# Optimization experiments

Measured on AMD Instinct MI355X. Metric: run time of the kernel, lower is better.

## Reference

```python
import jax, jax.numpy as jnp
import numpy as np

N_NODES = 50000
N_EDGES = 800000
FEATS = 128
HIDDEN = 64
CLASSES = 64


def graph_conv(x, edges):
    """GCN-style symmetric-normalized aggregation over an edge list (no self-loops;
    self information is supplied via the concat in the host module)."""
    src, dst = edges[0], edges[1]
    ones = jnp.ones((edges.shape[1],), dtype=x.dtype)
    deg = jax.ops.segment_sum(ones, dst, num_segments=N_NODES)
    inv_sqrt = jax.lax.rsqrt(jnp.maximum(deg, 1.0))
    coef = inv_sqrt[src] * inv_sqrt[dst]            # [E]
    msg = x[src] * coef[:, None]                     # [E, H] gather
    return jax.ops.segment_sum(msg, dst, num_segments=N_NODES)  # [N, H] scatter


def setup_inputs() -> dict:
    key = jax.random.key(0)
    ks = jax.random.split(key, 16)
    def lin(k, out_d, in_d):
        return jax.random.normal(k, (out_d, in_d), dtype=jnp.float32) / np.sqrt(in_d)
    x = jax.random.normal(ks[0], (N_NODES, FEATS), dtype=jnp.float32)
    edges = jax.random.randint(ks[1], (2, N_EDGES), 0, N_NODES, dtype=jnp.int64)
    return {
        "x": x,
        "edges": edges,
        "W1": lin(ks[2], HIDDEN, FEATS),
        "b1": jnp.zeros((HIDDEN,), dtype=jnp.float32),
        "W2": lin(ks[3], HIDDEN, 2 * HIDDEN),
        "A2a": lin(ks[4], HIDDEN, HIDDEN),
        "A2b": lin(ks[5], HIDDEN, HIDDEN),
        "W3": lin(ks[6], HIDDEN, 2 * HIDDEN),
        "A3a": lin(ks[7], HIDDEN, HIDDEN),
        "A3b": lin(ks[8], HIDDEN, HIDDEN),
        "W4": lin(ks[9], CLASSES, 2 * HIDDEN),
        "A4a": lin(ks[10], CLASSES, HIDDEN),
        "A4b": lin(ks[11], CLASSES, HIDDEN),
    }


def _block(x, edges, W, Aa, Ab):
    # relu(Linear(cat[x, conv(x)]) + att_a(x) * att_b(x))
    h = graph_conv(x, edges)
    cat = jnp.concatenate([x, h], axis=1)            # [N, 2H]
    return jax.nn.relu(cat @ W.T + (x @ Aa.T) * (x @ Ab.T))


def reference(x, edges, W1, b1, W2, A2a, A2b, W3, A3a, A3b, W4, A4a, A4b):
    x = jax.nn.relu(x @ W1.T + b1)                   # [N, H]
    x = _block(x, edges, W2, A2a, A2b)               # [N, H]
    x = _block(x, edges, W3, A3a, A3b)               # [N, H]
    x = _block(x, edges, W4, A4a, A4b)               # [N, C]
    return x
```

## Files before the change

kernel.cpp:

```cpp
#include <hip/hip_runtime.h>
#include <hip/hip_bf16.h>
#include <hip/hip_fp16.h>

#define N_NODES 50000
#define N_EDGES 800000
#define NTILES 3125
#define W_TOTAL 57344
#define WB2 192
#define SCAT 512
#define TB 782
#define ROWCAP 64
#define ZROW N_NODES

typedef __attribute__((ext_vector_type(8))) short bf16x8;
typedef __attribute__((ext_vector_type(4))) float f32x4;
typedef __attribute__((ext_vector_type(2))) float f32x2;
typedef __attribute__((ext_vector_type(8))) unsigned short u16x8;
typedef __attribute__((ext_vector_type(4))) unsigned int u32x4;

__device__ inline unsigned short f2bf(float f) {
    unsigned int x = __float_as_uint(f);
    unsigned int r = (x + 0x7FFF + ((x >> 16) & 1)) >> 16;
    return (unsigned short)r;
}
__device__ inline float2 h2f2(unsigned int u) {
    __half2 h = *(__half2*)&u;
    return make_float2(__low2float(h), __high2float(h));
}
__device__ inline unsigned int f22h2(float a, float b) {
    __half2 h = __floats2half2_rn(a, b);
    return *(unsigned int*)&h;
}

__global__ __launch_bounds__(256) void pass1_kernel(
    const float* __restrict__ x, const int* __restrict__ src, const int* __restrict__ dst,
    const float* __restrict__ W1, const float* __restrict__ b1,
    const float* W2, const float* A2a, const float* A2b,
    const float* W3, const float* A3a, const float* A3b,
    const float* W4, const float* A4a, const float* A4b,
    int* __restrict__ cnt, unsigned short* __restrict__ srcAp,
    unsigned short* __restrict__ wp, __half* __restrict__ Ht) {
    int tid = threadIdx.x;

    if (blockIdx.x < SCAT) {
        for (int e = blockIdx.x * 256 + tid; e < N_EDGES; e += SCAT * 256) {
            int d = dst[e];
            int pos = atomicAdd(&cnt[d], 1);
            if (pos < ROWCAP) srcAp[(size_t)d * ROWCAP + pos] = (unsigned short)src[e];
        }
        return;
    }
    if (blockIdx.x >= SCAT + TB) {
        int i = 8192 + (blockIdx.x - SCAT - TB) * 256 + tid;
        if (i >= W_TOTAL) return;
        float v;
        if (i < 16384)      v = W2[i - 8192];
        else if (i < 20480) v = A2a[i - 16384];
        else if (i < 24576) v = A2b[i - 20480];
        else if (i < 32768) v = W3[i - 24576];
        else if (i < 36864) v = A3a[i - 32768];
        else if (i < 40960) v = A3b[i - 36864];
        else if (i < 49152) v = W4[i - 40960];
        else if (i < 53248) v = A4a[i - 49152];
        else                v = A4b[i - 53248];
        wp[i] = f2bf(v);
        return;
    }

    int wave = ((blockIdx.x - SCAT) * 256 + tid) >> 6;
    if (wave >= NTILES) return;
    int lane = tid & 63;
    int r16 = lane & 15, quad = lane >> 4;
    int base = wave * 16;

    bf16x8 a[4];
    const float* xr = x + (size_t)(base + r16) * 128 + quad * 8;
#pragma unroll
    for (int kb = 0; kb < 4; kb++) {
        float4 f0 = *(const float4*)(xr + kb * 32);
        float4 f1 = *(const float4*)(xr + kb * 32 + 4);
        bf16x8 v;
        v[0] = (short)f2bf(f0.x); v[1] = (short)f2bf(f0.y);
        v[2] = (short)f2bf(f0.z); v[3] = (short)f2bf(f0.w);
        v[4] = (short)f2bf(f1.x); v[5] = (short)f2bf(f1.y);
        v[6] = (short)f2bf(f1.z); v[7] = (short)f2bf(f1.w);
        a[kb] = v;
    }

#pragma unroll
    for (int jt = 0; jt < 4; jt++) {
        f32x4 acc = {0.f, 0.f, 0.f, 0.f};
        const float* wr = W1 + (size_t)(jt * 16 + r16) * 128 + quad * 8;
#pragma unroll
        for (int kb = 0; kb < 4; kb++) {
            float4 g0 = *(const float4*)(wr + kb * 32);
            float4 g1 = *(const float4*)(wr + kb * 32 + 4);
            bf16x8 b;
            b[0] = (short)f2bf(g0.x); b[1] = (short)f2bf(g0.y);
            b[2] = (short)f2bf(g0.z); b[3] = (short)f2bf(g0.w);
            b[4] = (short)f2bf(g1.x); b[5] = (short)f2bf(g1.y);
            b[6] = (short)f2bf(g1.z); b[7] = (short)f2bf(g1.w);
            acc = __builtin_amdgcn_mfma_f32_16x16x32_bf16(a[kb], b, acc, 0, 0, 0);
        }
        int col = jt * 16 + r16;
        float bias = b1[col];
#pragma unroll
        for (int r = 0; r < 4; r++) {
            int row = base + quad * 4 + r;
            float v = fmaxf(acc[r] + bias, 0.f);
            Ht[(size_t)row * 64 + col] = __float2half(v);
        }
    }
}

__global__ __launch_bounds__(256) void scale_kernel(const int* __restrict__ cnt,
                                                    const __half* __restrict__ Ht,
                                                    __half* __restrict__ As,
                                                    unsigned char* __restrict__ As8,
                                                    unsigned short* __restrict__ srcAp,
                                                    float* __restrict__ isq,
                                                    float* __restrict__ sdeg) {
    int t = blockIdx.x * 256 + threadIdx.x;
    int row = t >> 4, sl = t & 15;
    if (row >= N_NODES) return;
    int c = cnt[row];
    float dv = fmaxf((float)c, 1.0f);
    float is = rsqrtf(dv);
    if (sl == 0) {
        isq[row] = is;
        sdeg[row] = sqrtf(dv);
    }
    int cv = min(c, ROWCAP);
    int cvr = (cv + 7) & ~7;
    if (sl < cvr - cv) srcAp[(size_t)row * ROWCAP + cv + sl] = (unsigned short)ZROW;

    uint2 rv = *((const uint2*)(Ht + (size_t)row * 64) + sl);
    float2 fa = h2f2(rv.x), fb = h2f2(rv.y);
    float s0 = fa.x * is, s1 = fa.y * is, s2 = fb.x * is, s3 = fb.y * is;
    uint2 ov;
    ov.x = f22h2(s0, s1);
    ov.y = f22h2(s2, s3);
    *((uint2*)(As + (size_t)row * 64) + sl) = ov;
    unsigned int w = __builtin_amdgcn_cvt_pk_fp8_f32(s0, s1, 0, false);
    w = __builtin_amdgcn_cvt_pk_fp8_f32(s2, s3, w, true);
    ((unsigned int*)As8)[(size_t)row * 16 + sl] = w;
}

__global__ __launch_bounds__(256) void conv_dense_k(const __half* __restrict__ hs,
                                                    const unsigned char* __restrict__ hs8,
                                                    const int* __restrict__ cnt,
                                                    const unsigned short* __restrict__ srcAp,
                                                    const float* __restrict__ isq,
                                                    const float* __restrict__ sdeg,
                                                    const unsigned short* __restrict__ wp,
                                                    const unsigned short* __restrict__ aap,
                                                    const unsigned short* __restrict__ abp,
                                                    __half* __restrict__ outs,
                                                    unsigned char* __restrict__ outs8,
                                                    float* __restrict__ outf,
                                                    int finalLayer) {
    __shared__ unsigned short clds[64][64];
    int tid = threadIdx.x;
    int wv = tid >> 6;
    int lane = tid & 63;
    int t = blockIdx.x * 4 + wv;
    if (t >= NTILES) return;
    int base = t * 16;

    {
        int r = lane >> 2, fl = lane & 3;
        int row = base + r;
        int b = row * ROWCAP;
        int cv = min(cnt[row], ROWCAP);
        int cvr = (cv + 7) & ~7;
        f32x2 acc[8];
#pragma unroll
        for (int k = 0; k < 8; k++) acc[k] = (f32x2){0.f, 0.f};
        if (cvr) {
            u16x8 sv = __builtin_nontemporal_load((const u16x8*)(srcAp + b));
            for (int i = 0; i < cvr; i += 8) {
                u16x8 svn = sv;
                if (i + 8 < cvr)
                    svn = __builtin_nontemporal_load((const u16x8*)(srcAp + b + i + 8));
                u32x4 rv[8];
#pragma unroll
                for (int u = 0; u < 8; u++)
                    rv[u] = *((const u32x4*)(hs8 + (size_t)(int)sv[u] * 64) + fl);
#pragma unroll
                for (int u = 0; u < 8; u++) {
                    acc[0] += __builtin_amdgcn_cvt_pk_f32_fp8(rv[u][0], false);
                    acc[1] += __builtin_amdgcn_cvt_pk_f32_fp8(rv[u][0], true);
                    acc[2] += __builtin_amdgcn_cvt_pk_f32_fp8(rv[u][1], false);
                    acc[3] += __builtin_amdgcn_cvt_pk_f32_fp8(rv[u][1], true);
                    acc[4] += __builtin_amdgcn_cvt_pk_f32_fp8(rv[u][2], false);
                    acc[5] += __builtin_amdgcn_cvt_pk_f32_fp8(rv[u][2], true);
                    acc[6] += __builtin_amdgcn_cvt_pk_f32_fp8(rv[u][3], false);
                    acc[7] += __builtin_amdgcn_cvt_pk_f32_fp8(rv[u][3], true);
                }
                sv = svn;
            }
        }
        float sc = isq[row];
        u16x8 o0, o1;
#pragma unroll
        for (int k = 0; k < 4; k++) {
            o0[2 * k]     = f2bf(acc[k][0] * sc);
            o0[2 * k + 1] = f2bf(acc[k][1] * sc);
            o1[2 * k]     = f2bf(acc[4 + k][0] * sc);
            o1[2 * k + 1] = f2bf(acc[4 + k][1] * sc);
        }
        *(u16x8*)(&clds[wv * 16 + r][fl * 16]) = o0;
        *(u16x8*)(&clds[wv * 16 + r][fl * 16 + 8]) = o1;
    }

    int r16 = lane & 15, quad = lane >> 4;
    float rs = sdeg[base + r16];
    const u32x4* hp = (const u32x4*)(hs + (size_t)(base + r16) * 64);
    u32x4 raw0 = __builtin_nontemporal_load(hp + quad);
    u32x4 raw1 = __builtin_nontemporal_load(hp + 4 + quad);
    bf16x8 ha0, ha1;
    {
        float2 f;
        f = h2f2(raw0[0]); ha0[0] = (short)f2bf(f.x * rs); ha0[1] = (short)f2bf(f.y * rs);
        f = h2f2(raw0[1]); ha0[2] = (short)f2bf(f.x * rs); ha0[3] = (short)f2bf(f.y * rs);
        f = h2f2(raw0[2]); ha0[4] = (short)f2bf(f.x * rs); ha0[5] = (short)f2bf(f.y * rs);
        f = h2f2(raw0[3]); ha0[6] = (short)f2bf(f.x * rs); ha0[7] = (short)f2bf(f.y * rs);
        f = h2f2(raw1[0]); ha1[0] = (short)f2bf(f.x * rs); ha1[1] = (short)f2bf(f.y * rs);
        f = h2f2(raw1[1]); ha1[2] = (short)f2bf(f.x * rs); ha1[3] = (short)f2bf(f.y * rs);
        f = h2f2(raw1[2]); ha1[4] = (short)f2bf(f.x * rs); ha1[5] = (short)f2bf(f.y * rs);
        f = h2f2(raw1[3]); ha1[6] = (short)f2bf(f.x * rs); ha1[7] = (short)f2bf(f.y * rs);
    }
    bf16x8 ca0 = *(const bf16x8*)(&clds[wv * 16 + r16][quad * 8]);
    bf16x8 ca1 = *(const bf16x8*)(&clds[wv * 16 + r16][32 + quad * 8]);

    float isq4[4];
    if (!finalLayer) {
#pragma unroll
        for (int r = 0; r < 4; r++) isq4[r] = isq[base + quad * 4 + r];
    }

#pragma unroll
    for (int jt = 0; jt < 4; jt++) {
        const unsigned short* wr = wp + (size_t)(jt * 16 + r16) * 128 + quad * 8;
        const unsigned short* ar = aap + (size_t)(jt * 16 + r16) * 64 + quad * 8;
        const unsigned short* br = abp + (size_t)(jt * 16 + r16) * 64 + quad * 8;
        f32x4 P = {0.f, 0.f, 0.f, 0.f};
        f32x4 Q = {0.f, 0.f, 0.f, 0.f};
        f32x4 R = {0.f, 0.f, 0.f, 0.f};
        P = __builtin_amdgcn_mfma_f32_16x16x32_bf16(ha0, *(const bf16x8*)(wr), P, 0, 0, 0);
        P = __builtin_amdgcn_mfma_f32_16x16x32_bf16(ha1, *(const bf16x8*)(wr + 32), P, 0, 0, 0);
        P = __builtin_amdgcn_mfma_f32_16x16x32_bf16(ca0, *(const bf16x8*)(wr + 64), P, 0, 0, 0);
        P = __builtin_amdgcn_mfma_f32_16x16x32_bf16(ca1, *(const bf16x8*)(wr + 96), P, 0, 0, 0);
        Q = __builtin_amdgcn_mfma_f32_16x16x32_bf16(ha0, *(const bf16x8*)(ar), Q, 0, 0, 0);
        Q = __builtin_amdgcn_mfma_f32_16x16x32_bf16(ha1, *(const bf16x8*)(ar + 32), Q, 0, 0, 0);
        R = __builtin_amdgcn_mfma_f32_16x16x32_bf16(ha0, *(const bf16x8*)(br), R, 0, 0, 0);
        R = __builtin_amdgcn_mfma_f32_16x16x32_bf16(ha1, *(const bf16x8*)(br + 32), R, 0, 0, 0);
        int col = jt * 16 + r16;
#pragma unroll
        for (int r = 0; r < 4; r++) {
            int row = base + quad * 4 + r;
            float v = fmaxf(P[r] + Q[r] * R[r], 0.f);
            if (finalLayer) {
                __builtin_nontemporal_store(v, &outf[(size_t)row * 64 + col]);
            } else {
                float vs = v * isq4[r];
                __half hv = __float2half(vs);
                __builtin_nontemporal_store(*(unsigned short*)&hv,
                                            (unsigned short*)outs + (size_t)row * 64 + col);
                unsigned int pb = __builtin_amdgcn_cvt_pk_fp8_f32(vs, vs, 0, false);
                outs8[(size_t)row * 64 + col] = (unsigned char)pb;
            }
        }
    }
}

extern "C" void kernel_launch(void* const* d_in, const int* in_sizes, int n_in,
                              void* d_out, int out_size, void* d_ws, size_t ws_size,
                              hipStream_t stream) {
    const float* x = (const float*)d_in[0];
    const int* edges = (const int*)d_in[1];
    const float* W1 = (const float*)d_in[2];
    const float* b1 = (const float*)d_in[3];
    const float* W2 = (const float*)d_in[4];
    const float* A2a = (const float*)d_in[5];
    const float* A2b = (const float*)d_in[6];
    const float* W3 = (const float*)d_in[7];
    const float* A3a = (const float*)d_in[8];
    const float* A3b = (const float*)d_in[9];
    const float* W4 = (const float*)d_in[10];
    const float* A4a = (const float*)d_in[11];
    const float* A4b = (const float*)d_in[12];
    float* out = (float*)d_out;

    const int* src = edges;
    const int* dst = edges + N_EDGES;

    char* p = (char*)d_ws;
    auto alloc = [&](size_t bytes) {
        char* r = p;
        p += (bytes + 255) & ~(size_t)255;
        return r;
    };
    int* cnt              = (int*)alloc(N_NODES * 4);
    float* isq            = (float*)alloc(N_NODES * 4);
    float* sdeg           = (float*)alloc(N_NODES * 4);
    unsigned short* srcAp = (unsigned short*)alloc((size_t)N_NODES * ROWCAP * 2);
    unsigned short* wpAll = (unsigned short*)alloc(W_TOTAL * 2);
    __half* Ht            = (__half*)alloc((size_t)N_NODES * 64 * 2);
    __half* As            = (__half*)alloc((size_t)N_NODES * 64 * 2);
    __half* Bs            = (__half*)alloc((size_t)N_NODES * 64 * 2);
    unsigned char* As8    = (unsigned char*)alloc((size_t)(N_NODES + 1) * 64);
    unsigned char* Bs8    = (unsigned char*)alloc((size_t)(N_NODES + 1) * 64);

    const unsigned short* W2p  = wpAll + 8192;
    const unsigned short* A2ap = wpAll + 16384;
    const unsigned short* A2bp = wpAll + 20480;
    const unsigned short* W3p  = wpAll + 24576;
    const unsigned short* A3ap = wpAll + 32768;
    const unsigned short* A3bp = wpAll + 36864;
    const unsigned short* W4p  = wpAll + 40960;
    const unsigned short* A4ap = wpAll + 49152;
    const unsigned short* A4bp = wpAll + 53248;

    hipMemsetAsync(cnt, 0, N_NODES * 4, stream);
    hipMemsetAsync(As8 + (size_t)ZROW * 64, 0, 64, stream);
    hipMemsetAsync(Bs8 + (size_t)ZROW * 64, 0, 64, stream);
    pass1_kernel<<<SCAT + TB + WB2, 256, 0, stream>>>(
        x, src, dst, W1, b1, W2, A2a, A2b, W3, A3a, A3b, W4, A4a, A4b,
        cnt, srcAp, wpAll, Ht);

    scale_kernel<<<(N_NODES * 16 + 255) / 256, 256, 0, stream>>>(
        cnt, Ht, As, As8, srcAp, isq, sdeg);

    conv_dense_k<<<TB, 256, 0, stream>>>(As, As8, cnt, srcAp, isq, sdeg,
                                         W2p, A2ap, A2bp, Bs, Bs8, nullptr, 0);
    conv_dense_k<<<TB, 256, 0, stream>>>(Bs, Bs8, cnt, srcAp, isq, sdeg,
                                         W3p, A3ap, A3bp, As, As8, nullptr, 0);
    conv_dense_k<<<TB, 256, 0, stream>>>(As, As8, cnt, srcAp, isq, sdeg,
                                         W4p, A4ap, A4bp, nullptr, nullptr, out, 1);
}
```

Before: 234.4 us.

## Privatize edge bucketing per XCD and compact adjacency lists in scale kernel

The edge scatter now reads the hardware XCC id and gives each of the eight XCDs its own private counter array and 16-slot adjacency buffer. It uses workgroup-scope relaxed atomics instead of device-wide atomics, aiming to keep atomic traffic inside the local L2 rather than crossing dies. The scale kernel then merges the eight sub-lists into a compacted per-row list, sums the degrees, and writes the final count. The trade-off is a memset eight times larger, extra merge work and memory traffic, and edges silently dropped when one XCD's share for a node exceeds 16. Workgroup-scope atomics are only safe if all blocks on one XCD share a coherent L2, which the code assumes.

```diff
diff --git a/kernel.cpp b/kernel.cpp
--- a/kernel.cpp
+++ b/kernel.cpp
@@ -10,6 +10,8 @@
 #define SCAT 512
 #define TB 782
 #define ROWCAP 64
+#define SUBCAP 16
+#define NXCD 8
 #define ZROW N_NODES
 
 typedef __attribute__((ext_vector_type(8))) short bf16x8;
@@ -38,15 +40,21 @@
     const float* W2, const float* A2a, const float* A2b,
     const float* W3, const float* A3a, const float* A3b,
     const float* W4, const float* A4a, const float* A4b,
-    int* __restrict__ cnt, unsigned short* __restrict__ srcAp,
+    int* __restrict__ cnt8, unsigned short* __restrict__ srcAp8,
     unsigned short* __restrict__ wp, __half* __restrict__ Ht) {
     int tid = threadIdx.x;
 
     if (blockIdx.x < SCAT) {
+        int xcc;
+        asm volatile("s_getreg_b32 %0, hwreg(HW_REG_XCC_ID)" : "=s"(xcc));
+        xcc &= (NXCD - 1);
+        int* mycnt = cnt8 + xcc * N_NODES;
+        unsigned short* myAp = srcAp8 + (size_t)xcc * N_NODES * SUBCAP;
         for (int e = blockIdx.x * 256 + tid; e < N_EDGES; e += SCAT * 256) {
             int d = dst[e];
-            int pos = atomicAdd(&cnt[d], 1);
-            if (pos < ROWCAP) srcAp[(size_t)d * ROWCAP + pos] = (unsigned short)src[e];
+            int pos = __hip_atomic_fetch_add(&mycnt[d], 1, __ATOMIC_RELAXED,
+                                             __HIP_MEMORY_SCOPE_WORKGROUP);
+            if (pos < SUBCAP) myAp[d * SUBCAP + pos] = (unsigned short)src[e];
         }
         return;
     }
@@ -113,26 +121,52 @@
     }
 }
 
-__global__ __launch_bounds__(256) void scale_kernel(const int* __restrict__ cnt,
+__global__ __launch_bounds__(256) void scale_kernel(const int* __restrict__ cnt8,
+                                                    int* __restrict__ cnt,
                                                     const __half* __restrict__ Ht,
                                                     __half* __restrict__ As,
                                                     unsigned char* __restrict__ As8,
-                                                    unsigned short* __restrict__ srcAp,
+                                                    const unsigned short* __restrict__ srcAp8,
+                                                    unsigned short* __restrict__ srcC,
                                                     float* __restrict__ isq,
                                                     float* __restrict__ sdeg) {
     int t = blockIdx.x * 256 + threadIdx.x;
     int row = t >> 4, sl = t & 15;
     if (row >= N_NODES) return;
-    int c = cnt[row];
-    float dv = fmaxf((float)c, 1.0f);
+
+    int deg = 0, total = 0;
+    int cv8[NXCD];
+#pragma unroll
+    for (int k = 0; k < NXCD; k++) {
+        int c = cnt8[k * N_NODES + row];
+        deg += c;
+        cv8[k] = min(c, SUBCAP);
+        total += cv8[k];
+    }
+    int x = sl & 7, h = sl >> 3;
+    int pfx = 0;
+#pragma unroll
+    for (int k = 0; k < NXCD; k++)
+        if (k < x) pfx += cv8[k];
+    int cv = min(total, ROWCAP);
+
+    int jend = min(cv8[x], h * 8 + 8);
+    for (int j = h * 8; j < jend; j++) {
+        int dpos = pfx + j;
+        if (dpos < ROWCAP)
+            srcC[(size_t)row * ROWCAP + dpos] =
+                srcAp8[(size_t)x * N_NODES * SUBCAP + (size_t)row * SUBCAP + j];
+    }
+    int cvr = (cv + 7) & ~7;
+    if (sl < cvr - cv) srcC[(size_t)row * ROWCAP + cv + sl] = (unsigned short)ZROW;
+
+    float dv = fmaxf((float)deg, 1.0f);
     float is = rsqrtf(dv);
     if (sl == 0) {
         isq[row] = is;
         sdeg[row] = sqrtf(dv);
-    }
-    int cv = min(c, ROWCAP);
-    int cvr = (cv + 7) & ~7;
-    if (sl < cvr - cv) srcAp[(size_t)row * ROWCAP + cv + sl] = (unsigned short)ZROW;
+        cnt[row] = cv;
+    }
 
     uint2 rv = *((const uint2*)(Ht + (size_t)row * 64) + sl);
     float2 fa = h2f2(rv.x), fb = h2f2(rv.y);
@@ -149,7 +183,7 @@
 __global__ __launch_bounds__(256) void conv_dense_k(const __half* __restrict__ hs,
                                                     const unsigned char* __restrict__ hs8,
                                                     const int* __restrict__ cnt,
-                                                    const unsigned short* __restrict__ srcAp,
+                                                    const unsigned short* __restrict__ srcC,
                                                     const float* __restrict__ isq,
                                                     const float* __restrict__ sdeg,
                                                     const unsigned short* __restrict__ wp,
@@ -177,11 +211,11 @@
 #pragma unroll
         for (int k = 0; k < 8; k++) acc[k] = (f32x2){0.f, 0.f};
         if (cvr) {
-            u16x8 sv = __builtin_nontemporal_load((const u16x8*)(srcAp + b));
+            u16x8 sv = __builtin_nontemporal_load((const u16x8*)(srcC + b));
             for (int i = 0; i < cvr; i += 8) {
                 u16x8 svn = sv;
                 if (i + 8 < cvr)
-                    svn = __builtin_nontemporal_load((const u16x8*)(srcAp + b + i + 8));
+                    svn = __builtin_nontemporal_load((const u16x8*)(srcC + b + i + 8));
                 u32x4 rv[8];
 #pragma unroll
                 for (int u = 0; u < 8; u++)
@@ -301,10 +335,12 @@
         p += (bytes + 255) & ~(size_t)255;
         return r;
     };
+    int* cnt8             = (int*)alloc((size_t)NXCD * N_NODES * 4);
     int* cnt              = (int*)alloc(N_NODES * 4);
     float* isq            = (float*)alloc(N_NODES * 4);
     float* sdeg           = (float*)alloc(N_NODES * 4);
-    unsigned short* srcAp = (unsigned short*)alloc((size_t)N_NODES * ROWCAP * 2);
+    unsigned short* srcAp8= (unsigned short*)alloc((size_t)NXCD * N_NODES * SUBCAP * 2);
+    unsigned short* srcC  = (unsigned short*)alloc((size_t)N_NODES * ROWCAP * 2);
     unsigned short* wpAll = (unsigned short*)alloc(W_TOTAL * 2);
     __half* Ht            = (__half*)alloc((size_t)N_NODES * 64 * 2);
     __half* As            = (__half*)alloc((size_t)N_NODES * 64 * 2);
@@ -322,20 +358,21 @@
     const unsigned short* A4ap = wpAll + 49152;
     const unsigned short* A4bp = wpAll + 53248;
 
-    hipMemsetAsync(cnt, 0, N_NODES * 4, stream);
+    hipMemsetAsync(cnt8, 0, (size_t)NXCD * N_NODES * 4, stream);
     hipMemsetAsync(As8 + (size_t)ZROW * 64, 0, 64, stream);
     hipMemsetAsync(Bs8 + (size_t)ZROW * 64, 0, 64, stream);
+
     pass1_kernel<<<SCAT + TB + WB2, 256, 0, stream>>>(
         x, src, dst, W1, b1, W2, A2a, A2b, W3, A3a, A3b, W4, A4a, A4b,
-        cnt, srcAp, wpAll, Ht);
+        cnt8, srcAp8, wpAll, Ht);
 
     scale_kernel<<<(N_NODES * 16 + 255) / 256, 256, 0, stream>>>(
-        cnt, Ht, As, As8, srcAp, isq, sdeg);
-
-    conv_dense_k<<<TB, 256, 0, stream>>>(As, As8, cnt, srcAp, isq, sdeg,
+        cnt8, cnt, Ht, As, As8, srcAp8, srcC, isq, sdeg);
+
+    conv_dense_k<<<TB, 256, 0, stream>>>(As, As8, cnt, srcC, isq, sdeg,
                                          W2p, A2ap, A2bp, Bs, Bs8, nullptr, 0);
-    conv_dense_k<<<TB, 256, 0, stream>>>(Bs, Bs8, cnt, srcAp, isq, sdeg,
+    conv_dense_k<<<TB, 256, 0, stream>>>(Bs, Bs8, cnt, srcC, isq, sdeg,
                                          W3p, A3ap, A3bp, As, As8, nullptr, 0);
-    conv_dense_k<<<TB, 256, 0, stream>>>(As, As8, cnt, srcAp, isq, sdeg,
+    conv_dense_k<<<TB, 256, 0, stream>>>(As, As8, cnt, srcC, isq, sdeg,
                                          W4p, A4ap, A4bp, nullptr, nullptr, out, 1);
 }
```

Measured after the change: 233.5 us. About the same (-0.4%).

## Replace global per-node atomic scatter with two-level bucketed CSR build

Applied to the files above, without the earlier changes.

Edges are first binned into 200 destination buckets, using shared-memory histograms and one global atomic per bucket per block. A new csr_k kernel then builds the per-node source lists inside each bucket with shared-memory atomics, and does the ZROW padding and degree write that scale_kernel used to do. The aim is to replace 800K contended global atomics and scattered writes with local atomics and more coalesced writes. The cost is an extra kernel launch, an extra pass over the edges, a bucket capacity cap (4400 entries) that could drop edges, and a new limit that source indices must fit in 16 bits.

```diff
diff --git a/kernel.cpp b/kernel.cpp
--- a/kernel.cpp
+++ b/kernel.cpp
@@ -7,10 +7,15 @@
 #define NTILES 3125
 #define W_TOTAL 57344
 #define WB2 192
-#define SCAT 512
 #define TB 782
 #define ROWCAP 64
 #define ZROW N_NODES
+
+#define NBKT 200
+#define BKT_NODES 250
+#define BKT_CAP 4400
+#define ABLK 256
+#define ACH ((N_EDGES + ABLK - 1) / ABLK)
 
 typedef __attribute__((ext_vector_type(8))) short bf16x8;
 typedef __attribute__((ext_vector_type(4))) float f32x4;
@@ -32,26 +37,44 @@
     return *(unsigned int*)&h;
 }
 
-__global__ __launch_bounds__(256) void pass1_kernel(
+__global__ __launch_bounds__(256) void passA_kernel(
     const float* __restrict__ x, const int* __restrict__ src, const int* __restrict__ dst,
     const float* __restrict__ W1, const float* __restrict__ b1,
     const float* W2, const float* A2a, const float* A2b,
     const float* W3, const float* A3a, const float* A3b,
     const float* W4, const float* A4a, const float* A4b,
-    int* __restrict__ cnt, unsigned short* __restrict__ srcAp,
+    int* __restrict__ bucketCnt, unsigned int* __restrict__ bktArr,
     unsigned short* __restrict__ wp, __half* __restrict__ Ht) {
     int tid = threadIdx.x;
 
-    if (blockIdx.x < SCAT) {
-        for (int e = blockIdx.x * 256 + tid; e < N_EDGES; e += SCAT * 256) {
+    if (blockIdx.x < ABLK) {
+        __shared__ int hist[NBKT];
+        __shared__ int gbase[NBKT];
+        __shared__ int hoff[NBKT];
+        if (tid < NBKT) { hist[tid] = 0; hoff[tid] = 0; }
+        __syncthreads();
+        int e0 = blockIdx.x * ACH;
+        int e1 = min(e0 + ACH, N_EDGES);
+        for (int e = e0 + tid; e < e1; e += 256)
+            atomicAdd(&hist[dst[e] / BKT_NODES], 1);
+        __syncthreads();
+        if (tid < NBKT) {
+            int h = hist[tid];
+            gbase[tid] = h ? atomicAdd(&bucketCnt[tid], h) : 0;
+        }
+        __syncthreads();
+        for (int e = e0 + tid; e < e1; e += 256) {
             int d = dst[e];
-            int pos = atomicAdd(&cnt[d], 1);
-            if (pos < ROWCAP) srcAp[(size_t)d * ROWCAP + pos] = (unsigned short)src[e];
+            int b = d / BKT_NODES;
+            int pos = gbase[b] + atomicAdd(&hoff[b], 1);
+            if (pos < BKT_CAP)
+                bktArr[(size_t)b * BKT_CAP + pos] =
+                    ((unsigned int)(d - b * BKT_NODES) << 16) | (unsigned int)src[e];
         }
         return;
     }
-    if (blockIdx.x >= SCAT + TB) {
-        int i = 8192 + (blockIdx.x - SCAT - TB) * 256 + tid;
+    if (blockIdx.x >= ABLK + TB) {
+        int i = 8192 + (blockIdx.x - ABLK - TB) * 256 + tid;
         if (i >= W_TOTAL) return;
         float v;
         if (i < 16384)      v = W2[i - 8192];
@@ -67,7 +90,7 @@
         return;
     }
 
-    int wave = ((blockIdx.x - SCAT) * 256 + tid) >> 6;
+    int wave = ((blockIdx.x - ABLK) * 256 + tid) >> 6;
     if (wave >= NTILES) return;
     int lane = tid & 63;
     int r16 = lane & 15, quad = lane >> 4;
@@ -113,27 +136,50 @@
     }
 }
 
+__global__ __launch_bounds__(256) void csr_k(const int* __restrict__ bucketCnt,
+                                             const unsigned int* __restrict__ bktArr,
+                                             unsigned short* __restrict__ srcAp,
+                                             int* __restrict__ cnt) {
+    __shared__ int lcnt[BKT_NODES];
+    int b = blockIdx.x, tid = threadIdx.x;
+    if (tid < BKT_NODES) lcnt[tid] = 0;
+    __syncthreads();
+    int n = min(bucketCnt[b], BKT_CAP);
+    int rowbase = b * BKT_NODES;
+    const unsigned int* arr = bktArr + (size_t)b * BKT_CAP;
+    for (int i = tid; i < n; i += 256) {
+        unsigned int u = arr[i];
+        int dl = (int)(u >> 16);
+        int pos = atomicAdd(&lcnt[dl], 1);
+        if (pos < ROWCAP)
+            srcAp[(size_t)(rowbase + dl) * ROWCAP + pos] = (unsigned short)(u & 0xFFFF);
+    }
+    __syncthreads();
+    if (tid < BKT_NODES) {
+        int deg = lcnt[tid];
+        int cv = min(deg, ROWCAP);
+        int cvr = (cv + 7) & ~7;
+        for (int j = cv; j < cvr; j++)
+            srcAp[(size_t)(rowbase + tid) * ROWCAP + j] = (unsigned short)ZROW;
+        cnt[rowbase + tid] = deg;
+    }
+}
+
 __global__ __launch_bounds__(256) void scale_kernel(const int* __restrict__ cnt,
                                                     const __half* __restrict__ Ht,
                                                     __half* __restrict__ As,
                                                     unsigned char* __restrict__ As8,
-                                                    unsigned short* __restrict__ srcAp,
                                                     float* __restrict__ isq,
                                                     float* __restrict__ sdeg) {
     int t = blockIdx.x * 256 + threadIdx.x;
     int row = t >> 4, sl = t & 15;
     if (row >= N_NODES) return;
-    int c = cnt[row];
-    float dv = fmaxf((float)c, 1.0f);
+    float dv = fmaxf((float)cnt[row], 1.0f);
     float is = rsqrtf(dv);
     if (sl == 0) {
         isq[row] = is;
         sdeg[row] = sqrtf(dv);
     }
-    int cv = min(c, ROWCAP);
-    int cvr = (cv + 7) & ~7;
-    if (sl < cvr - cv) srcAp[(size_t)row * ROWCAP + cv + sl] = (unsigned short)ZROW;
-
     uint2 rv = *((const uint2*)(Ht + (size_t)row * 64) + sl);
     float2 fa = h2f2(rv.x), fb = h2f2(rv.y);
     float s0 = fa.x * is, s1 = fa.y * is, s2 = fb.x * is, s3 = fb.y * is;
@@ -301,6 +347,8 @@
         p += (bytes + 255) & ~(size_t)255;
         return r;
     };
+    int* bucketCnt        = (int*)alloc(NBKT * 4);
+    unsigned int* bktArr  = (unsigned int*)alloc((size_t)NBKT * BKT_CAP * 4);
     int* cnt              = (int*)alloc(N_NODES * 4);
     float* isq            = (float*)alloc(N_NODES * 4);
     float* sdeg           = (float*)alloc(N_NODES * 4);
@@ -322,15 +370,18 @@
     const unsigned short* A4ap = wpAll + 49152;
     const unsigned short* A4bp = wpAll + 53248;
 
-    hipMemsetAsync(cnt, 0, N_NODES * 4, stream);
+    hipMemsetAsync(bucketCnt, 0, NBKT * 4, stream);
     hipMemsetAsync(As8 + (size_t)ZROW * 64, 0, 64, stream);
     hipMemsetAsync(Bs8 + (size_t)ZROW * 64, 0, 64, stream);
-    pass1_kernel<<<SCAT + TB + WB2, 256, 0, stream>>>(
+
+    passA_kernel<<<ABLK + TB + WB2, 256, 0, stream>>>(
         x, src, dst, W1, b1, W2, A2a, A2b, W3, A3a, A3b, W4, A4a, A4b,
-        cnt, srcAp, wpAll, Ht);
+        bucketCnt, bktArr, wpAll, Ht);
+
+    csr_k<<<NBKT, 256, 0, stream>>>(bucketCnt, bktArr, srcAp, cnt);
 
     scale_kernel<<<(N_NODES * 16 + 255) / 256, 256, 0, stream>>>(
-        cnt, Ht, As, As8, srcAp, isq, sdeg);
+        cnt, Ht, As, As8, isq, sdeg);
 
     conv_dense_k<<<TB, 256, 0, stream>>>(As, As8, cnt, srcAp, isq, sdeg,
                                          W2p, A2ap, A2bp, Bs, Bs8, nullptr, 0);
```

Result: faster. 226.9 us (-3.2%).
